# Performance work log

Measured on AMD Instinct MI355X. Metric: run time of the kernel, lower is better.

The kernel has to match this reference:

```python
import jax, jax.numpy as jnp
import numpy as np

N_NODES = 100000
N_EDGES = 1600000
IN_CH = 128
OUT_CH = 64
HID = 2 * OUT_CH  # 128


def _gcn_conv(x, src, dst, deg_inv_sqrt, W, b, n_nodes):
    """PyG GCNConv with symmetric normalization; self-loops already in (src, dst)."""
    h = x @ W                                   # [N, F_out] dense GEMM
    norm = deg_inv_sqrt[src] * deg_inv_sqrt[dst]  # [E+N]
    msg = h[src] * norm[:, None]                # gather + scale (irregular)
    out = jax.ops.segment_sum(msg, dst, num_segments=n_nodes)  # scatter-add
    return out + b


def setup_inputs() -> dict:
    key = jax.random.key(0)
    ks = jax.random.split(key, 8)
    x = jax.random.normal(ks[0], (N_NODES, IN_CH), dtype=jnp.float32)
    edge_index = jax.random.randint(ks[1], (2, N_EDGES), 0, N_NODES, dtype=jnp.int64)
    # Glorot-ish params for the three GCNConv layers
    W1 = jax.random.normal(ks[2], (IN_CH, HID), dtype=jnp.float32) / np.sqrt(IN_CH)
    b1 = jnp.zeros((HID,), dtype=jnp.float32)
    W_mu = jax.random.normal(ks[3], (HID, OUT_CH), dtype=jnp.float32) / np.sqrt(HID)
    b_mu = jnp.zeros((OUT_CH,), dtype=jnp.float32)
    W_ls = jax.random.normal(ks[4], (HID, OUT_CH), dtype=jnp.float32) / np.sqrt(HID)
    b_ls = jnp.zeros((OUT_CH,), dtype=jnp.float32)
    return {"x": x, "edge_index": edge_index, "W1": W1, "b1": b1,
            "W_mu": W_mu, "b_mu": b_mu, "W_ls": W_ls, "b_ls": b_ls}


def reference(x, edge_index, W1, b1, W_mu, b_mu, W_ls, b_ls):
    n = x.shape[0]
    # GCNConv adds self-loops to the same edge_index in every layer; do it once.
    loop = jnp.arange(n, dtype=edge_index.dtype)
    src = jnp.concatenate([edge_index[0], loop])  # source / row
    dst = jnp.concatenate([edge_index[1], loop])  # target / col
    # Symmetric normalization: deg over targets with unit edge weights.
    deg = jax.ops.segment_sum(jnp.ones_like(dst, dtype=x.dtype), dst, num_segments=n)
    deg_inv_sqrt = jnp.where(deg > 0, jax.lax.rsqrt(jnp.maximum(deg, 1.0)), 0.0)

    h = jax.nn.relu(_gcn_conv(x, src, dst, deg_inv_sqrt, W1, b1, n))
    mu = _gcn_conv(h, src, dst, deg_inv_sqrt, W_mu, b_mu, n)
    logstd = _gcn_conv(h, src, dst, deg_inv_sqrt, W_ls, b_ls, n)
    return mu, logstd
```

## Files before the change

### kernel.cpp

```cpp
#include <hip/hip_runtime.h>
#include <hip/hip_bf16.h>
#include <stdint.h>


static inline size_t align_up(size_t x, size_t a) { return (x + a - 1) / a * a; }

typedef __attribute__((ext_vector_type(8))) short short8;
typedef __attribute__((ext_vector_type(4))) float f32x4;

#define BSHIFT 7
#define BNODES 128
#define CHUNKS 512
#define NBMAX 1024

__device__ inline unsigned short f2bf(float f) {
    unsigned u = __float_as_uint(f);
    unsigned r = (u + 0x7FFFu + ((u >> 16) & 1u)) >> 16;
    return (unsigned short)r;
}
__device__ inline float bf2f(unsigned v16) {
    return __uint_as_float(v16 << 16);
}

__device__ inline bool detect_i64_local(const void* ei, int lo, int hi, int t) {
    __shared__ int s_nz;
    if (t == 0) s_nz = 0;
    __syncthreads();
    int nz = 0;
    int lim = min(hi, lo + 1024);
    const int* p = (const int*)ei;
    for (int i = lo + t; i < lim; i += 256) {
        if (p[2 * i + 1] != 0) nz = 1;
    }
    if (nz) atomicOr(&s_nz, 1);
    __syncthreads();
    return s_nz == 0;
}

__device__ inline int load_idx2(const void* ei, bool is64, size_t pos, int n) {
    int v;
    if (is64) v = (int)((const long long*)ei)[pos];
    else      v = ((const int*)ei)[pos];
    return (v < 0) ? 0 : (v >= n ? n - 1 : v);
}


__global__ __launch_bounds__(256) void chunk_hist_kernel(
        const void* __restrict__ ei, int* __restrict__ hmat,
        int E, int n, int nb, int epc) {
    __shared__ int hist[NBMAX];
    const int c = blockIdx.x, t = threadIdx.x;
    const int lo = min(E, c * epc), hi = min(E, lo + epc);
    bool is64 = detect_i64_local(ei, lo, hi, t);
    for (int i = t; i < nb; i += 256) hist[i] = 0;
    __syncthreads();
    for (int i = lo + t; i < hi; i += 256) {
        int d = load_idx2(ei, is64, (size_t)E + i, n);
        atomicAdd(&hist[d >> BSHIFT], 1);
    }
    __syncthreads();
    for (int i = t; i < nb; i += 256) hmat[(size_t)c * nb + i] = hist[i];
}


__global__ __launch_bounds__(256) void bucket_scan_cols_kernel(
        int* __restrict__ hmat, int* __restrict__ btot, int nb) {
    __shared__ int tmp[256];
    const int b = blockIdx.x, t = threadIdx.x;
    const int c0 = 2 * t;
    int va = hmat[(size_t)c0 * nb + b];
    int vb = hmat[(size_t)(c0 + 1) * nb + b];
    int pair = va + vb;
    tmp[t] = pair;
    __syncthreads();
    for (int off = 1; off < 256; off <<= 1) {
        int u = (t >= off) ? tmp[t - off] : 0;
        __syncthreads();
        tmp[t] += u;
        __syncthreads();
    }
    int excl = tmp[t] - pair;
    hmat[(size_t)c0 * nb + b] = excl;
    hmat[(size_t)(c0 + 1) * nb + b] = excl + va;
    if (t == 255) btot[b] = tmp[255];
}


__global__ void base_scan_kernel(const int* __restrict__ btot, int* __restrict__ bbase, int nb) {
    __shared__ int tmp[NBMAX];
    int t = threadIdx.x;
    int v = (t < nb) ? btot[t] : 0;
    tmp[t] = v;
    __syncthreads();
    for (int off = 1; off < NBMAX; off <<= 1) {
        int u = (t >= off) ? tmp[t - off] : 0;
        __syncthreads();
        tmp[t] += u;
        __syncthreads();
    }
    if (t < nb) bbase[t] = tmp[t] - v;
}


__global__ __launch_bounds__(256) void chunk_scatter_kernel(
        const void* __restrict__ ei, const int* __restrict__ hmat,
        const int* __restrict__ bbase, unsigned* __restrict__ binned,
        int E, int n, int nb, int epc) {
    __shared__ int lcur[NBMAX];
    const int c = blockIdx.x, t = threadIdx.x;
    const int lo = min(E, c * epc), hi = min(E, lo + epc);
    bool is64 = detect_i64_local(ei, lo, hi, t);
    for (int i = t; i < nb; i += 256) lcur[i] = hmat[(size_t)c * nb + i] + bbase[i];
    __syncthreads();
    for (int i = lo + t; i < hi; i += 256) {
        int s = load_idx2(ei, is64, i, n);
        int d = load_idx2(ei, is64, (size_t)E + i, n);
        int b = d >> BSHIFT;
        int pos = atomicAdd(&lcur[b], 1);
        binned[pos] = ((unsigned)s << BSHIFT) | (unsigned)(d & (BNODES - 1));
    }
}


__global__ __launch_bounds__(256) void bucket_csr_kernel(
        const unsigned* __restrict__ binned, const int* __restrict__ bbase,
        const int* __restrict__ btot, float* __restrict__ dis,
        int* __restrict__ row_beg, int* __restrict__ row_end,
        int* __restrict__ csr_src, int n) {
    __shared__ int ldeg[BNODES];
    __shared__ int lscan[BNODES];
    __shared__ int lcur[BNODES];
    const int b = blockIdx.x;
    const int t = threadIdx.x;
    const int base = bbase[b];
    const int cnt = btot[b];

    if (t < BNODES) ldeg[t] = 0;
    __syncthreads();
    for (int i = t; i < cnt; i += 256) {
        unsigned w = binned[base + i];
        atomicAdd(&ldeg[w & (BNODES - 1)], 1);
    }
    __syncthreads();
    int v = (t < BNODES) ? ldeg[t] : 0;
    if (t < BNODES) lscan[t] = v;
    __syncthreads();
    for (int off = 1; off < BNODES; off <<= 1) {
        int u = (t < BNODES && t >= off) ? lscan[t - off] : 0;
        __syncthreads();
        if (t < BNODES) lscan[t] += u;
        __syncthreads();
    }
    if (t < BNODES) {
        int excl = lscan[t] - v;
        lcur[t] = excl;
        int node = (b << BSHIFT) + t;
        if (node < n) {
            dis[node] = rsqrtf((float)v + 1.0f);
            row_beg[node] = base + excl;
            row_end[node] = base + excl + v;
        }
    }
    __syncthreads();
    for (int i = t; i < cnt; i += 256) {
        unsigned w = binned[base + i];
        int pos = atomicAdd(&lcur[w & (BNODES - 1)], 1);
        csr_src[base + pos] = (int)(w >> BSHIFT);
    }
}


__global__ void prep_weights_kernel(const float* __restrict__ W1,
                                    const float* __restrict__ Wmu,
                                    const float* __restrict__ Wls,
                                    unsigned short* __restrict__ Wt1,
                                    unsigned short* __restrict__ Wtcat) {
    int idx = blockIdx.x * 256 + threadIdx.x;
    if (idx < 16384) {
        int c = idx >> 7, k = idx & 127;
        Wt1[c * 128 + k] = f2bf(W1[k * 128 + c]);
    } else if (idx < 32768) {
        int i = idx - 16384;
        int j = i >> 7, k = i & 127;
        float v = (j < 64) ? Wmu[k * 64 + j] : Wls[k * 64 + (j - 64)];
        Wtcat[j * 128 + k] = f2bf(v);
    }
}


template <int MODE>
__global__ __launch_bounds__(256) void mfma_gemm_kernel(
        const void* __restrict__ Ax, const unsigned short* __restrict__ Wt,
        const float* __restrict__ biasA, const float* __restrict__ biasB,
        void* __restrict__ outA, void* __restrict__ outB, int n) {
    __shared__ unsigned short ws[128 * 136];
    const int tid = threadIdx.x;
    const int wave = tid >> 6, lane = tid & 63;
    const int brow = blockIdx.x * 64 + wave * 16;
    const int lr = lane & 15;
    const int kg = lane >> 4;
    const int k0 = kg * 8;

    for (int i = tid; i < 2048; i += 256) {
        int r = i >> 4, ci = i & 15;
        *(short8*)&ws[r * 136 + ci * 8] = *(const short8*)&Wt[r * 128 + ci * 8];
    }
    __syncthreads();

    int arow = brow + lr;
    if (arow >= n) arow = n - 1;

    f32x4 acc[8];
#pragma unroll
    for (int t = 0; t < 8; ++t) acc[t] = (f32x4){0.f, 0.f, 0.f, 0.f};

#pragma unroll
    for (int c = 0; c < 4; ++c) {
        short8 a;
        if (MODE == 0) {
            const float* ap = (const float*)Ax + (size_t)arow * 128 + c * 32 + k0;
            float4 lo = *(const float4*)ap;
            float4 hi = *(const float4*)(ap + 4);
            a[0] = (short)f2bf(lo.x); a[1] = (short)f2bf(lo.y);
            a[2] = (short)f2bf(lo.z); a[3] = (short)f2bf(lo.w);
            a[4] = (short)f2bf(hi.x); a[5] = (short)f2bf(hi.y);
            a[6] = (short)f2bf(hi.z); a[7] = (short)f2bf(hi.w);
        } else {
            a = *(const short8*)((const unsigned short*)Ax + (size_t)arow * 128 + c * 32 + k0);
        }
#pragma unroll
        for (int t = 0; t < 8; ++t) {
            short8 bfr = *(const short8*)&ws[(t * 16 + lr) * 136 + c * 32 + k0];
            acc[t] = __builtin_amdgcn_mfma_f32_16x16x32_bf16(a, bfr, acc[t], 0, 0, 0);
        }
    }

    if (MODE == 0) {
        unsigned short* out = (unsigned short*)outA;
#pragma unroll
        for (int t = 0; t < 8; ++t) {
            int col = t * 16 + lr;
#pragma unroll
            for (int r = 0; r < 4; ++r) {
                int row = brow + kg * 4 + r;
                if (row < n) out[(size_t)row * 128 + col] = f2bf(acc[t][r]);
            }
        }
    } else {
        float* oA = (float*)outA;
        float* oB = (float*)outB;
#pragma unroll
        for (int t = 0; t < 8; ++t) {
            int col = t * 16 + lr;
            float bv = (col < 64) ? biasA[col] : biasB[col - 64];
#pragma unroll
            for (int r = 0; r < 4; ++r) {
                int row = brow + kg * 4 + r;
                if (row < n) {
                    float v = acc[t][r] + bv;
                    if (col < 64) oA[(size_t)row * 64 + col] = v;
                    else          oB[(size_t)row * 64 + (col - 64)] = v;
                }
            }
        }
    }
}


__global__ __launch_bounds__(256) void csr_agg_kernel(
        const unsigned short* __restrict__ hin, const int* __restrict__ row_beg,
        const int* __restrict__ row_end, const int* __restrict__ csr_src,
        const float* __restrict__ dis, const float* __restrict__ bias,
        unsigned short* __restrict__ out, int n, int relu) {
    int node = blockIdx.x * 4 + (threadIdx.x >> 6);
    if (node >= n) return;
    const int lane = threadIdx.x & 63;
    const int hi_half = lane >> 5;
    const unsigned foff = (lane & 31) * 8;
    int beg = row_beg[node], end = row_end[node];
    float dv = dis[node];

    const char* hinb = (const char*)hin;

    float a0x = 0.f, a0y = 0.f, a0z = 0.f, a0w = 0.f;
    float a1x = 0.f, a1y = 0.f, a1z = 0.f, a1w = 0.f;
    float a2x = 0.f, a2y = 0.f, a2z = 0.f, a2w = 0.f;
    float a3x = 0.f, a3y = 0.f, a3z = 0.f, a3w = 0.f;

    int e = beg;
    for (; e + 7 < end; e += 8) {
        int s0 = csr_src[e + 0 + hi_half];
        int s1 = csr_src[e + 2 + hi_half];
        int s2 = csr_src[e + 4 + hi_half];
        int s3 = csr_src[e + 6 + hi_half];
        float w0 = dis[s0], w1 = dis[s1], w2 = dis[s2], w3 = dis[s3];
        uint2 d0 = *(const uint2*)(hinb + (size_t)s0 * 256 + foff);
        uint2 d1 = *(const uint2*)(hinb + (size_t)s1 * 256 + foff);
        uint2 d2 = *(const uint2*)(hinb + (size_t)s2 * 256 + foff);
        uint2 d3 = *(const uint2*)(hinb + (size_t)s3 * 256 + foff);
        a0x += bf2f(d0.x & 0xffffu) * w0; a0y += bf2f(d0.x >> 16) * w0;
        a0z += bf2f(d0.y & 0xffffu) * w0; a0w += bf2f(d0.y >> 16) * w0;
        a1x += bf2f(d1.x & 0xffffu) * w1; a1y += bf2f(d1.x >> 16) * w1;
        a1z += bf2f(d1.y & 0xffffu) * w1; a1w += bf2f(d1.y >> 16) * w1;
        a2x += bf2f(d2.x & 0xffffu) * w2; a2y += bf2f(d2.x >> 16) * w2;
        a2z += bf2f(d2.y & 0xffffu) * w2; a2w += bf2f(d2.y >> 16) * w2;
        a3x += bf2f(d3.x & 0xffffu) * w3; a3y += bf2f(d3.x >> 16) * w3;
        a3z += bf2f(d3.y & 0xffffu) * w3; a3w += bf2f(d3.y >> 16) * w3;
    }
    for (; e + 1 < end; e += 2) {
        int s = csr_src[e + hi_half];
        float w = dis[s];
        uint2 d = *(const uint2*)(hinb + (size_t)s * 256 + foff);
        a0x += bf2f(d.x & 0xffffu) * w; a0y += bf2f(d.x >> 16) * w;
        a0z += bf2f(d.y & 0xffffu) * w; a0w += bf2f(d.y >> 16) * w;
    }
    if (e < end) {
        int s = csr_src[e];
        float w = 0.5f * dis[s];
        uint2 d = *(const uint2*)(hinb + (size_t)s * 256 + foff);
        a1x += bf2f(d.x & 0xffffu) * w; a1y += bf2f(d.x >> 16) * w;
        a1z += bf2f(d.y & 0xffffu) * w; a1w += bf2f(d.y >> 16) * w;
    }

    float sx = (a0x + a1x) + (a2x + a3x);
    float sy = (a0y + a1y) + (a2y + a3y);
    float sz = (a0z + a1z) + (a2z + a3z);
    float sw = (a0w + a1w) + (a2w + a3w);
    sx += __shfl_xor(sx, 32, 64);
    sy += __shfl_xor(sy, 32, 64);
    sz += __shfl_xor(sz, 32, 64);
    sw += __shfl_xor(sw, 32, 64);

    uint2 sd = *(const uint2*)(hinb + (size_t)node * 256 + foff);
    sx = dv * (sx + dv * bf2f(sd.x & 0xffffu));
    sy = dv * (sy + dv * bf2f(sd.x >> 16));
    sz = dv * (sz + dv * bf2f(sd.y & 0xffffu));
    sw = dv * (sw + dv * bf2f(sd.y >> 16));

    if (bias) {
        float4 bb = *(const float4*)&bias[(lane & 31) * 4];
        sx += bb.x; sy += bb.y; sz += bb.z; sw += bb.w;
    }
    if (relu) {
        sx = fmaxf(sx, 0.f); sy = fmaxf(sy, 0.f);
        sz = fmaxf(sz, 0.f); sw = fmaxf(sw, 0.f);
    }
    if (lane < 32) {
        uint2 o;
        o.x = (unsigned)f2bf(sx) | ((unsigned)f2bf(sy) << 16);
        o.y = (unsigned)f2bf(sz) | ((unsigned)f2bf(sw) << 16);
        *(uint2*)((char*)out + (size_t)node * 256 + foff) = o;
    }
}


extern "C" void kernel_launch(void* const* d_in, const int* in_sizes, int n_in,
                              void* d_out, int out_size, void* d_ws, size_t ws_size,
                              hipStream_t stream) {
    const float* x   = (const float*)d_in[0];
    const void*  ei  = d_in[1];
    const float* W1  = (const float*)d_in[2];
    const float* b1  = (const float*)d_in[3];
    const float* Wmu = (const float*)d_in[4];
    const float* bmu = (const float*)d_in[5];
    const float* Wls = (const float*)d_in[6];
    const float* bls = (const float*)d_in[7];

    const int n = in_sizes[0] / 128;
    const int E = in_sizes[1] / 2;
    const int nb = (n + BNODES - 1) >> BSHIFT;
    const int epc = (E + CHUNKS - 1) / CHUNKS;

    float* out   = (float*)d_out;
    float* outMu = out;
    float* outLs = out + (size_t)n * 64;

    char* w = (char*)d_ws;
    auto alloc = [&](size_t bytes) { char* p = w; w += align_up(bytes, 256); return p; };
    int*            hmat    = (int*)           alloc((size_t)CHUNKS * nb * 4);
    int*            btot    = (int*)           alloc(NBMAX * 4);
    int*            bbase   = (int*)           alloc(NBMAX * 4);
    unsigned*       binned  = (unsigned*)      alloc((size_t)E * 4);
    int*            row_beg = (int*)           alloc((size_t)n * 4);
    int*            row_end = (int*)           alloc((size_t)n * 4);
    float*          dis     = (float*)         alloc((size_t)n * 4);
    int*            csr_src = (int*)           alloc((size_t)E * 4);
    unsigned short* Wt1     = (unsigned short*)alloc(128 * 128 * 2);
    unsigned short* Wtcat   = (unsigned short*)alloc(128 * 128 * 2);
    unsigned short* xW      = (unsigned short*)alloc((size_t)n * 128 * 2);
    unsigned short* h       = (unsigned short*)alloc((size_t)n * 128 * 2);
    unsigned short* hagg    = (unsigned short*)alloc((size_t)n * 128 * 2);

    chunk_hist_kernel<<<CHUNKS, 256, 0, stream>>>(ei, hmat, E, n, nb, epc);
    bucket_scan_cols_kernel<<<nb, 256, 0, stream>>>(hmat, btot, nb);
    base_scan_kernel<<<1, NBMAX, 0, stream>>>(btot, bbase, nb);
    chunk_scatter_kernel<<<CHUNKS, 256, 0, stream>>>(ei, hmat, bbase, binned, E, n, nb, epc);
    bucket_csr_kernel<<<nb, 256, 0, stream>>>(binned, bbase, btot, dis, row_beg, row_end,
                                              csr_src, n);
    prep_weights_kernel<<<128, 256, 0, stream>>>(W1, Wmu, Wls, Wt1, Wtcat);

    const int gblocks = (n + 63) / 64;

    mfma_gemm_kernel<0><<<gblocks, 256, 0, stream>>>(x, Wt1, nullptr, nullptr, xW, nullptr, n);
    csr_agg_kernel<<<(n + 3) / 4, 256, 0, stream>>>(xW, row_beg, row_end, csr_src,
                                                    dis, b1, h, n, 1);

    csr_agg_kernel<<<(n + 3) / 4, 256, 0, stream>>>(h, row_beg, row_end, csr_src,
                                                    dis, nullptr, hagg, n, 0);
    mfma_gemm_kernel<1><<<gblocks, 256, 0, stream>>>(hagg, Wtcat, bmu, bls, outMu, outLs, n);
}
```

Measured before the change: 236.7 us.

## Fuse first GEMM with edge histogram and convert weights inside GEMM kernels

The first dense GEMM (x@W1) and the per-chunk destination histogram now run in one launch, with different block ranges doing each job, so the independent GEMM can overlap the CSR build front-end. The separate weight-prep kernel is removed: each GEMM block transposes and converts its fp32 weights to bf16 into LDS itself. This drops two launches and one dependency, but every block now redoes the 16K-element strided weight conversion from global memory, and the shared-memory footprint of the histogram blocks grows to that of the GEMM blocks.

```diff
diff --git a/kernel.cpp b/kernel.cpp
--- a/kernel.cpp
+++ b/kernel.cpp
@@ -45,21 +45,73 @@
 }
 
 
-__global__ __launch_bounds__(256) void chunk_hist_kernel(
+__global__ __launch_bounds__(256) void front_kernel(
+        const float* __restrict__ x, const float* __restrict__ W1,
+        unsigned short* __restrict__ xW, int n, int gblocks,
         const void* __restrict__ ei, int* __restrict__ hmat,
-        int E, int n, int nb, int epc) {
-    __shared__ int hist[NBMAX];
-    const int c = blockIdx.x, t = threadIdx.x;
-    const int lo = min(E, c * epc), hi = min(E, lo + epc);
-    bool is64 = detect_i64_local(ei, lo, hi, t);
-    for (int i = t; i < nb; i += 256) hist[i] = 0;
-    __syncthreads();
-    for (int i = lo + t; i < hi; i += 256) {
-        int d = load_idx2(ei, is64, (size_t)E + i, n);
-        atomicAdd(&hist[d >> BSHIFT], 1);
-    }
-    __syncthreads();
-    for (int i = t; i < nb; i += 256) hmat[(size_t)c * nb + i] = hist[i];
+        int E, int nb, int epc) {
+    __shared__ unsigned short ws[128 * 136];
+    const int tid = threadIdx.x;
+
+    if ((int)blockIdx.x < gblocks) {
+        const int wave = tid >> 6, lane = tid & 63;
+        const int brow = blockIdx.x * 64 + wave * 16;
+        const int lr = lane & 15;
+        const int kg = lane >> 4;
+        const int k0 = kg * 8;
+
+        for (int i = tid; i < 16384; i += 256) {
+            int k = i >> 7, c = i & 127;
+            ws[c * 136 + k] = f2bf(W1[k * 128 + c]);
+        }
+        __syncthreads();
+
+        int arow = brow + lr;
+        if (arow >= n) arow = n - 1;
+
+        f32x4 acc[8];
+#pragma unroll
+        for (int t = 0; t < 8; ++t) acc[t] = (f32x4){0.f, 0.f, 0.f, 0.f};
+
+#pragma unroll
+        for (int c = 0; c < 4; ++c) {
+            const float* ap = x + (size_t)arow * 128 + c * 32 + k0;
+            float4 lo = *(const float4*)ap;
+            float4 hi = *(const float4*)(ap + 4);
+            short8 a;
+            a[0] = (short)f2bf(lo.x); a[1] = (short)f2bf(lo.y);
+            a[2] = (short)f2bf(lo.z); a[3] = (short)f2bf(lo.w);
+            a[4] = (short)f2bf(hi.x); a[5] = (short)f2bf(hi.y);
+            a[6] = (short)f2bf(hi.z); a[7] = (short)f2bf(hi.w);
+#pragma unroll
+            for (int t = 0; t < 8; ++t) {
+                short8 bfr = *(const short8*)&ws[(t * 16 + lr) * 136 + c * 32 + k0];
+                acc[t] = __builtin_amdgcn_mfma_f32_16x16x32_bf16(a, bfr, acc[t], 0, 0, 0);
+            }
+        }
+#pragma unroll
+        for (int t = 0; t < 8; ++t) {
+            int col = t * 16 + lr;
+#pragma unroll
+            for (int r = 0; r < 4; ++r) {
+                int row = brow + kg * 4 + r;
+                if (row < n) xW[(size_t)row * 128 + col] = f2bf(acc[t][r]);
+            }
+        }
+    } else {
+        int* hist = (int*)ws;
+        const int c = blockIdx.x - gblocks;
+        const int lo = min(E, c * epc), hi = min(E, lo + epc);
+        bool is64 = detect_i64_local(ei, lo, hi, tid);
+        for (int i = tid; i < nb; i += 256) hist[i] = 0;
+        __syncthreads();
+        for (int i = lo + tid; i < hi; i += 256) {
+            int d = load_idx2(ei, is64, (size_t)E + i, n);
+            atomicAdd(&hist[d >> BSHIFT], 1);
+        }
+        __syncthreads();
+        for (int i = tid; i < nb; i += 256) hmat[(size_t)c * nb + i] = hist[i];
+    }
 }
 
 
@@ -170,29 +222,11 @@
 }
 
 
-__global__ void prep_weights_kernel(const float* __restrict__ W1,
-                                    const float* __restrict__ Wmu,
-                                    const float* __restrict__ Wls,
-                                    unsigned short* __restrict__ Wt1,
-                                    unsigned short* __restrict__ Wtcat) {
-    int idx = blockIdx.x * 256 + threadIdx.x;
-    if (idx < 16384) {
-        int c = idx >> 7, k = idx & 127;
-        Wt1[c * 128 + k] = f2bf(W1[k * 128 + c]);
-    } else if (idx < 32768) {
-        int i = idx - 16384;
-        int j = i >> 7, k = i & 127;
-        float v = (j < 64) ? Wmu[k * 64 + j] : Wls[k * 64 + (j - 64)];
-        Wtcat[j * 128 + k] = f2bf(v);
-    }
-}
-
-
-template <int MODE>
-__global__ __launch_bounds__(256) void mfma_gemm_kernel(
-        const void* __restrict__ Ax, const unsigned short* __restrict__ Wt,
-        const float* __restrict__ biasA, const float* __restrict__ biasB,
-        void* __restrict__ outA, void* __restrict__ outB, int n) {
+__global__ __launch_bounds__(256) void gemm2_kernel(
+        const unsigned short* __restrict__ hagg,
+        const float* __restrict__ Wmu, const float* __restrict__ Wls,
+        const float* __restrict__ bmu, const float* __restrict__ bls,
+        float* __restrict__ outMu, float* __restrict__ outLs, int n) {
     __shared__ unsigned short ws[128 * 136];
     const int tid = threadIdx.x;
     const int wave = tid >> 6, lane = tid & 63;
@@ -201,9 +235,10 @@
     const int kg = lane >> 4;
     const int k0 = kg * 8;
 
-    for (int i = tid; i < 2048; i += 256) {
-        int r = i >> 4, ci = i & 15;
-        *(short8*)&ws[r * 136 + ci * 8] = *(const short8*)&Wt[r * 128 + ci * 8];
+    for (int i = tid; i < 16384; i += 256) {
+        int k = i >> 7, c = i & 127;
+        float v = (c < 64) ? Wmu[k * 64 + c] : Wls[k * 64 + (c - 64)];
+        ws[c * 136 + k] = f2bf(v);
     }
     __syncthreads();
 
@@ -216,18 +251,7 @@
 
 #pragma unroll
     for (int c = 0; c < 4; ++c) {
-        short8 a;
-        if (MODE == 0) {
-            const float* ap = (const float*)Ax + (size_t)arow * 128 + c * 32 + k0;
-            float4 lo = *(const float4*)ap;
-            float4 hi = *(const float4*)(ap + 4);
-            a[0] = (short)f2bf(lo.x); a[1] = (short)f2bf(lo.y);
-            a[2] = (short)f2bf(lo.z); a[3] = (short)f2bf(lo.w);
-            a[4] = (short)f2bf(hi.x); a[5] = (short)f2bf(hi.y);
-            a[6] = (short)f2bf(hi.z); a[7] = (short)f2bf(hi.w);
-        } else {
-            a = *(const short8*)((const unsigned short*)Ax + (size_t)arow * 128 + c * 32 + k0);
-        }
+        short8 a = *(const short8*)(hagg + (size_t)arow * 128 + c * 32 + k0);
 #pragma unroll
         for (int t = 0; t < 8; ++t) {
             short8 bfr = *(const short8*)&ws[(t * 16 + lr) * 136 + c * 32 + k0];
@@ -235,32 +259,17 @@
         }
     }
 
-    if (MODE == 0) {
-        unsigned short* out = (unsigned short*)outA;
-#pragma unroll
-        for (int t = 0; t < 8; ++t) {
-            int col = t * 16 + lr;
-#pragma unroll
-            for (int r = 0; r < 4; ++r) {
-                int row = brow + kg * 4 + r;
-                if (row < n) out[(size_t)row * 128 + col] = f2bf(acc[t][r]);
-            }
-        }
-    } else {
-        float* oA = (float*)outA;
-        float* oB = (float*)outB;
-#pragma unroll
-        for (int t = 0; t < 8; ++t) {
-            int col = t * 16 + lr;
-            float bv = (col < 64) ? biasA[col] : biasB[col - 64];
-#pragma unroll
-            for (int r = 0; r < 4; ++r) {
-                int row = brow + kg * 4 + r;
-                if (row < n) {
-                    float v = acc[t][r] + bv;
-                    if (col < 64) oA[(size_t)row * 64 + col] = v;
-                    else          oB[(size_t)row * 64 + (col - 64)] = v;
-                }
+#pragma unroll
+    for (int t = 0; t < 8; ++t) {
+        int col = t * 16 + lr;
+        float bv = (col < 64) ? bmu[col] : bls[col - 64];
+#pragma unroll
+        for (int r = 0; r < 4; ++r) {
+            int row = brow + kg * 4 + r;
+            if (row < n) {
+                float v = acc[t][r] + bv;
+                if (col < 64) outMu[(size_t)row * 64 + col] = v;
+                else          outLs[(size_t)row * 64 + (col - 64)] = v;
             }
         }
     }
@@ -385,27 +394,25 @@
     int*            row_end = (int*)           alloc((size_t)n * 4);
     float*          dis     = (float*)         alloc((size_t)n * 4);
     int*            csr_src = (int*)           alloc((size_t)E * 4);
-    unsigned short* Wt1     = (unsigned short*)alloc(128 * 128 * 2);
-    unsigned short* Wtcat   = (unsigned short*)alloc(128 * 128 * 2);
     unsigned short* xW      = (unsigned short*)alloc((size_t)n * 128 * 2);
     unsigned short* h       = (unsigned short*)alloc((size_t)n * 128 * 2);
     unsigned short* hagg    = (unsigned short*)alloc((size_t)n * 128 * 2);
 
-    chunk_hist_kernel<<<CHUNKS, 256, 0, stream>>>(ei, hmat, E, n, nb, epc);
+    const int gblocks = (n + 63) / 64;
+
+    front_kernel<<<gblocks + CHUNKS, 256, 0, stream>>>(x, W1, xW, n, gblocks,
+                                                       ei, hmat, E, nb, epc);
+
     bucket_scan_cols_kernel<<<nb, 256, 0, stream>>>(hmat, btot, nb);
     base_scan_kernel<<<1, NBMAX, 0, stream>>>(btot, bbase, nb);
     chunk_scatter_kernel<<<CHUNKS, 256, 0, stream>>>(ei, hmat, bbase, binned, E, n, nb, epc);
     bucket_csr_kernel<<<nb, 256, 0, stream>>>(binned, bbase, btot, dis, row_beg, row_end,
                                               csr_src, n);
-    prep_weights_kernel<<<128, 256, 0, stream>>>(W1, Wmu, Wls, Wt1, Wtcat);
-
-    const int gblocks = (n + 63) / 64;
-
-    mfma_gemm_kernel<0><<<gblocks, 256, 0, stream>>>(x, Wt1, nullptr, nullptr, xW, nullptr, n);
+
     csr_agg_kernel<<<(n + 3) / 4, 256, 0, stream>>>(xW, row_beg, row_end, csr_src,
                                                     dis, b1, h, n, 1);
 
     csr_agg_kernel<<<(n + 3) / 4, 256, 0, stream>>>(h, row_beg, row_end, csr_src,
                                                     dis, nullptr, hagg, n, 0);
-    mfma_gemm_kernel<1><<<gblocks, 256, 0, stream>>>(hagg, Wtcat, bmu, bls, outMu, outLs, n);
-}
+    gemm2_kernel<<<gblocks, 256, 0, stream>>>(hagg, Wmu, Wls, bmu, bls, outMu, outLs, n);
+}
```

New measurement: 239.2 us. Within noise of the previous version (+1.1%).
